# Kernel tuning notes

Hardware: AMD Instinct MI355X
Metric: run time of the kernel (lower is better)

The kernel has to match this reference:

```python
import jax, jax.numpy as jnp
import numpy as np

EPS = 1e-12  # torch F.normalize default eps


def setup_inputs() -> dict:
    key = jax.random.key(0)
    k1, k2, k3, k4, k5 = jax.random.split(key, 5)
    N, E, D_IN, D_OUT = 100000, 1600000, 128, 128
    features = jax.random.normal(k1, (N, D_IN), dtype=jnp.float32)
    W = jax.random.normal(k2, (D_OUT, D_IN), dtype=jnp.float32) * 0.05
    b = jax.random.normal(k3, (D_OUT,), dtype=jnp.float32) * 0.05
    src = jax.random.randint(k4, (E,), 0, N, dtype=jnp.int32)
    dst = jax.random.randint(k5, (E,), 0, N, dtype=jnp.int32)
    return {"features": features, "W": W, "b": b, "src": src, "dst": dst}


def reference(features, W, b, src, dst):
    N = features.shape[0]
    # sum of features over each node's neighbors: scatter-add messages to dst
    neigh_sum = jax.ops.segment_sum(features[src], dst, num_segments=N)  # [N, D]
    total = jnp.sum(features, axis=0)  # [D]
    # non-neighbor sum (excl. self) + self feature == total - neighbor_sum
    h_NN = total[None, :] - neigh_sum  # [N, D]
    # row-wise L2 normalize (torch F.normalize dim=1)
    norm = jnp.sqrt(jnp.sum(h_NN * h_NN, axis=1, keepdims=True))
    h_norm = h_NN / jnp.maximum(norm, EPS)
    # linear: x @ W.T + b
    return h_norm @ W.T + b
```

## Files before the change

kernel.cpp:

```cpp
#include <hip/hip_runtime.h>
#include <hip/hip_bf16.h>

#define D 128

typedef __bf16 bf16_t;
typedef bf16_t bf16x8 __attribute__((ext_vector_type(8)));
typedef float  f32x4  __attribute__((ext_vector_type(4)));
typedef float  f32x2  __attribute__((ext_vector_type(2)));

__device__ __forceinline__ void atomAddF(float* p, float v) {
    unsafeAtomicAdd(p, v);
}

__device__ __forceinline__ uint2 pack_fp8x8(const float* v) {
    unsigned lo = 0, hi = 0;
    lo = __builtin_amdgcn_cvt_pk_fp8_f32(v[0], v[1], lo, false);
    lo = __builtin_amdgcn_cvt_pk_fp8_f32(v[2], v[3], lo, true);
    hi = __builtin_amdgcn_cvt_pk_fp8_f32(v[4], v[5], hi, false);
    hi = __builtin_amdgcn_cvt_pk_fp8_f32(v[6], v[7], hi, true);
    return make_uint2(lo, hi);
}

__device__ __forceinline__ void acc_fp8x8(uint2 w, float* acc) {
    f32x2 a = __builtin_amdgcn_cvt_pk_f32_fp8(w.x, false);
    f32x2 b = __builtin_amdgcn_cvt_pk_f32_fp8(w.x, true);
    f32x2 c = __builtin_amdgcn_cvt_pk_f32_fp8(w.y, false);
    f32x2 d = __builtin_amdgcn_cvt_pk_f32_fp8(w.y, true);
    acc[0] += a[0]; acc[1] += a[1]; acc[2] += b[0]; acc[3] += b[1];
    acc[4] += c[0]; acc[5] += c[1]; acc[6] += d[0]; acc[7] += d[1];
}

__global__ __launch_bounds__(256) void cvt_colsum_count_kernel(const float* __restrict__ feat,
                                                               uint2* __restrict__ featq,
                                                               float* __restrict__ total,
                                                               const int* __restrict__ dst,
                                                               int* __restrict__ bcount,
                                                               long long n8, int nE, int NB) {
    __shared__ float red[4][16][8];
    __shared__ int hist[1024];
    int tid = threadIdx.x, lane = tid & 63, w = tid >> 6;
    for (int i = tid; i < NB; i += 256) hist[i] = 0;
    __syncthreads();
    long long G = (long long)gridDim.x * 256;
    float acc[8];
    #pragma unroll
    for (int e = 0; e < 8; ++e) acc[e] = 0.f;
    long long lim = n8 > (long long)nE ? n8 : (long long)nE;
    for (long long i = (long long)blockIdx.x * 256 + tid; i < lim; i += G) {
        if (i < n8) {
            const float4 a = *(const float4*)&feat[i * 8];
            const float4 b = *(const float4*)&feat[i * 8 + 4];
            float v[8] = {a.x, a.y, a.z, a.w, b.x, b.y, b.z, b.w};
            featq[i] = pack_fp8x8(v);
            acc[0] += a.x; acc[1] += a.y; acc[2] += a.z; acc[3] += a.w;
            acc[4] += b.x; acc[5] += b.y; acc[6] += b.z; acc[7] += b.w;
        }
        if (i < (long long)nE) atomicAdd(&hist[dst[i] >> 8], 1);
    }
    #pragma unroll
    for (int e = 0; e < 8; ++e) {
        acc[e] += __shfl_xor(acc[e], 16, 64);
        acc[e] += __shfl_xor(acc[e], 32, 64);
    }
    if (lane < 16) {
        #pragma unroll
        for (int e = 0; e < 8; ++e) red[w][lane][e] = acc[e];
    }
    __syncthreads();
    if (tid < 128) {
        int cb = tid >> 3, e = tid & 7;
        float s = red[0][cb][e] + red[1][cb][e] + red[2][cb][e] + red[3][cb][e];
        atomAddF(&total[cb * 8 + e], s);
    }
    for (int i = tid; i < NB; i += 256) {
        int h = hist[i];
        if (h) atomicAdd(&bcount[i], h);
    }
}

__global__ __launch_bounds__(1024) void bscan_kernel(const int* __restrict__ bcount,
                                                     int* __restrict__ bbase,
                                                     int* __restrict__ bcur,
                                                     int NB, int nE) {
    int tid = threadIdx.x, lane = tid & 63, w = tid >> 6;
    int v = (tid < NB) ? bcount[tid] : 0;
    int x = v;
    #pragma unroll
    for (int off = 1; off < 64; off <<= 1) {
        int y = __shfl_up(x, off, 64);
        if (lane >= off) x += y;
    }
    __shared__ int ws[16];
    if (lane == 63) ws[w] = x;
    __syncthreads();
    if (w == 0 && lane < 16) {
        int s = ws[lane];
        #pragma unroll
        for (int off = 1; off < 16; off <<= 1) {
            int y = __shfl_up(s, off, 64);
            if (lane >= off) s += y;
        }
        ws[lane] = s;
    }
    __syncthreads();
    int base = (w == 0) ? 0 : ws[w - 1];
    int excl = base + x - v;
    if (tid < NB) { bbase[tid] = excl; bcur[tid] = excl; }
    if (tid == 0) bbase[NB] = nE;
}

__global__ __launch_bounds__(256) void bucket_scatter_kernel(const int* __restrict__ src,
                                                             const int* __restrict__ dst,
                                                             int* __restrict__ bcur,
                                                             unsigned* __restrict__ packed,
                                                             int nE, int NB, int chunk) {
    __shared__ int hist[1024];
    __shared__ int cur[1024];
    int tid = threadIdx.x;
    int c0 = blockIdx.x * chunk;
    int c1 = c0 + chunk; if (c1 > nE) c1 = nE;
    for (int i = tid; i < NB; i += 256) hist[i] = 0;
    __syncthreads();
    for (int i = c0 + tid; i < c1; i += 256) atomicAdd(&hist[dst[i] >> 8], 1);
    __syncthreads();
    for (int i = tid; i < NB; i += 256) {
        int h = hist[i];
        cur[i] = h ? atomicAdd(&bcur[i], h) : 0;
    }
    __syncthreads();
    for (int i = c0 + tid; i < c1; i += 256) {
        int t = dst[i];
        int b = t >> 8;
        int off = atomicAdd(&cur[b], 1);
        packed[off] = ((unsigned)(t & 255) << 17) | (unsigned)src[i];
    }
}

__global__ __launch_bounds__(512) void fill_sort_kernel(const unsigned* __restrict__ packed,
                                                        const int* __restrict__ bbase,
                                                        int* __restrict__ ptr,
                                                        int* __restrict__ adj,
                                                        int n, int NB, int nE) {
    __shared__ int cnt[256];
    __shared__ int lcur[256];
    __shared__ int wsum[4];
    int b = blockIdx.x;
    int tid = threadIdx.x, lane = tid & 63, w = tid >> 6;
    int base = bbase[b], end = bbase[b + 1];
    if (tid < 256) cnt[tid] = 0;
    __syncthreads();
    for (int i = base + tid; i < end; i += 512)
        atomicAdd(&cnt[packed[i] >> 17], 1);
    __syncthreads();
    int v = 0, x = 0;
    if (tid < 256) {
        v = cnt[tid];
        x = v;
        #pragma unroll
        for (int off = 1; off < 64; off <<= 1) {
            int y = __shfl_up(x, off, 64);
            if (lane >= off) x += y;
        }
        if (lane == 63) wsum[w] = x;
    }
    __syncthreads();
    if (tid < 256) {
        int wb = 0;
        for (int k = 0; k < w; ++k) wb += wsum[k];
        int excl = wb + x - v;
        int start = base + excl;
        lcur[tid] = start;
        int node = b * 256 + tid;
        if (node < n) ptr[node] = start;
    }
    if (b == NB - 1 && tid == 0) ptr[n] = nE;
    __syncthreads();
    for (int i = base + tid; i < end; i += 512) {
        unsigned pv = packed[i];
        int j = (int)(pv >> 17);
        int pos = atomicAdd(&lcur[j], 1);
        adj[pos] = (int)(pv & 0x1FFFFu);
    }
}

__global__ __launch_bounds__(256, 4) void gather_mfma_kernel(const uint2* __restrict__ featq,
                                                             const int* __restrict__ ptr,
                                                             const int* __restrict__ adj,
                                                             const float* __restrict__ total,
                                                             const float* __restrict__ W,
                                                             const float* __restrict__ bias,
                                                             float* __restrict__ out,
                                                             int n, int ngroups) {
    __shared__ bf16_t s_hn[2][16][136];

    int tid  = threadIdx.x;
    int lane = tid & 63;
    int w    = tid >> 6;
    int quad = lane >> 4;
    int l16  = lane & 15;

    int n0 = w * 32;
    bf16x8 bfrag[4][2];
    #pragma unroll
    for (int s = 0; s < 4; ++s)
        #pragma unroll
        for (int c = 0; c < 2; ++c) {
            const float* wp = W + (size_t)(n0 + 16 * c + l16) * D + 32 * s + 8 * quad;
            float4 wa = *(const float4*)wp;
            float4 wb = *(const float4*)(wp + 4);
            bf16x8 bf;
            bf[0] = (bf16_t)wa.x; bf[1] = (bf16_t)wa.y; bf[2] = (bf16_t)wa.z; bf[3] = (bf16_t)wa.w;
            bf[4] = (bf16_t)wb.x; bf[5] = (bf16_t)wb.y; bf[6] = (bf16_t)wb.z; bf[7] = (bf16_t)wb.w;
            bfrag[s][c] = bf;
        }
    float bias0 = bias[n0 + l16];
    float bias1 = bias[n0 + 16 + l16];

    int k_node = tid >> 4;
    int d8 = (tid & 15) * 8;
    float tot8[8];
    {
        float4 ta = *(const float4*)&total[d8];
        float4 tb = *(const float4*)&total[d8 + 4];
        tot8[0] = ta.x; tot8[1] = ta.y; tot8[2] = ta.z; tot8[3] = ta.w;
        tot8[4] = tb.x; tot8[5] = tb.y; tot8[6] = tb.z; tot8[7] = tb.w;
    }

    const uint2* fb = featq + (tid & 15);
    int pb = 0;

    for (int g = blockIdx.x; g < ngroups; g += gridDim.x) {
        int v = g * 16 + k_node;
        bool valid = v < n;
        int p0 = valid ? ptr[v] : 0;
        int p1 = valid ? ptr[v + 1] : 0;

        float acc8[8];
        #pragma unroll
        for (int e = 0; e < 8; ++e) acc8[e] = 0.f;

        for (int p = p0; p < p1; p += 16) {
            int rem = p1 - p;
            uint2 f[16];
            #pragma unroll
            for (int i = 0; i < 16; ++i) {
                int q = (i < rem) ? (p + i) : (p1 - 1);
                f[i] = fb[(size_t)adj[q] * 16];
            }
            #pragma unroll
            for (int i = 0; i < 16; ++i) {
                if (i < rem) acc_fp8x8(f[i], acc8);
            }
        }

        float h8[8], ss = 0.f;
        #pragma unroll
        for (int e = 0; e < 8; ++e) {
            h8[e] = valid ? (tot8[e] - acc8[e]) : 0.f;
            ss = fmaf(h8[e], h8[e], ss);
        }
        ss += __shfl_xor(ss, 1, 64);
        ss += __shfl_xor(ss, 2, 64);
        ss += __shfl_xor(ss, 4, 64);
        ss += __shfl_xor(ss, 8, 64);
        float rinv = 1.0f / fmaxf(sqrtf(ss), 1e-12f);

        bf16x8 hv;
        #pragma unroll
        for (int e = 0; e < 8; ++e) hv[e] = (bf16_t)(h8[e] * rinv);
        *(bf16x8*)&s_hn[pb][k_node][d8] = hv;
        __syncthreads();

        f32x4 acc0 = {0.f, 0.f, 0.f, 0.f};
        f32x4 acc1 = {0.f, 0.f, 0.f, 0.f};
        #pragma unroll
        for (int s = 0; s < 4; ++s) {
            bf16x8 a = *(const bf16x8*)&s_hn[pb][l16][32 * s + 8 * quad];
            acc0 = __builtin_amdgcn_mfma_f32_16x16x32_bf16(a, bfrag[s][0], acc0, 0, 0, 0);
            acc1 = __builtin_amdgcn_mfma_f32_16x16x32_bf16(a, bfrag[s][1], acc1, 0, 0, 0);
        }
        #pragma unroll
        for (int r = 0; r < 4; ++r) {
            int row = quad * 4 + r;
            int vr = g * 16 + row;
            if (vr < n) {
                out[(size_t)vr * D + n0 + l16]      = acc0[r] + bias0;
                out[(size_t)vr * D + n0 + 16 + l16] = acc1[r] + bias1;
            }
        }
        pb ^= 1;
    }
}

__global__ __launch_bounds__(128) void col_sum_kernel(const float* __restrict__ feat,
                                                      float* __restrict__ total, int n) {
    int d = threadIdx.x;
    float acc = 0.f;
    for (int r = blockIdx.x; r < n; r += gridDim.x)
        acc += feat[(size_t)r * D + d];
    atomAddF(&total[d], acc);
}

__global__ __launch_bounds__(256) void scatter_kernel(const float* __restrict__ feat,
                                                      const int* __restrict__ src,
                                                      const int* __restrict__ dst,
                                                      float* __restrict__ neigh, int nE) {
    long long nwork = (long long)nE * 64;
    long long stride = (long long)gridDim.x * 256;
    for (long long i = (long long)blockIdx.x * 256 + threadIdx.x; i < nwork; i += stride) {
        int e = (int)(i >> 6);
        int d2 = (int)(i & 63) * 2;
        int s = src[e], t = dst[e];
        const float2 vv = *(const float2*)&feat[(size_t)s * D + d2];
        float* p = &neigh[(size_t)t * D + d2];
        atomAddF(p + 0, vv.x);
        atomAddF(p + 1, vv.y);
    }
}

__global__ __launch_bounds__(256) void finalize_kernel(const float* __restrict__ neigh,
                                                       const float* __restrict__ total,
                                                       const float* __restrict__ W,
                                                       const float* __restrict__ bias,
                                                       float* __restrict__ out,
                                                       int n, int ngroups) {
    __shared__ __hip_bfloat16 Wt[D * D];
    __shared__ __align__(16) float hnt[2][D][4];
    __shared__ float red[2][2][4];
    int tid = threadIdx.x;
    for (int idx = tid; idx < D * D; idx += 256) {
        int j = idx & 127, dd = idx >> 7;
        Wt[idx] = __float2bfloat16(W[(size_t)j * D + dd]);
    }
    int half = tid >> 7, d = tid & 127, wih = (tid >> 6) & 1, lane = tid & 63;
    float bj = bias[d], tot = total[d];
    __syncthreads();
    for (int g = blockIdx.x; g < ngroups; g += gridDim.x) {
        int nb = g * 8 + half * 4;
        float h0=0,h1=0,h2=0,h3=0;
        if (nb+0 < n) h0 = tot - neigh[(size_t)(nb+0)*D + d];
        if (nb+1 < n) h1 = tot - neigh[(size_t)(nb+1)*D + d];
        if (nb+2 < n) h2 = tot - neigh[(size_t)(nb+2)*D + d];
        if (nb+3 < n) h3 = tot - neigh[(size_t)(nb+3)*D + d];
        float s0=h0*h0,s1=h1*h1,s2=h2*h2,s3=h3*h3;
        #pragma unroll
        for (int off = 32; off > 0; off >>= 1) {
            s0 += __shfl_xor(s0, off, 64); s1 += __shfl_xor(s1, off, 64);
            s2 += __shfl_xor(s2, off, 64); s3 += __shfl_xor(s3, off, 64);
        }
        if (lane == 0) { red[half][wih][0]=s0; red[half][wih][1]=s1; red[half][wih][2]=s2; red[half][wih][3]=s3; }
        __syncthreads();
        float rinv[4];
        #pragma unroll
        for (int k = 0; k < 4; ++k)
            rinv[k] = 1.0f / fmaxf(sqrtf(red[half][0][k] + red[half][1][k]), 1e-12f);
        hnt[half][d][0]=h0*rinv[0]; hnt[half][d][1]=h1*rinv[1];
        hnt[half][d][2]=h2*rinv[2]; hnt[half][d][3]=h3*rinv[3];
        __syncthreads();
        float a0=0,a1=0,a2=0,a3=0;
        #pragma unroll 8
        for (int dd = 0; dd < D; ++dd) {
            float4 hn4 = *(const float4*)&hnt[half][dd][0];
            float wv = __bfloat162float(Wt[dd * D + d]);
            a0 = fmaf(hn4.x, wv, a0); a1 = fmaf(hn4.y, wv, a1);
            a2 = fmaf(hn4.z, wv, a2); a3 = fmaf(hn4.w, wv, a3);
        }
        if (nb+0 < n) out[(size_t)(nb+0)*D + d] = a0 + bj;
        if (nb+1 < n) out[(size_t)(nb+1)*D + d] = a1 + bj;
        if (nb+2 < n) out[(size_t)(nb+2)*D + d] = a2 + bj;
        if (nb+3 < n) out[(size_t)(nb+3)*D + d] = a3 + bj;
        __syncthreads();
    }
}

static inline size_t align_up(size_t x, size_t a) { return (x + a - 1) & ~(a - 1); }

extern "C" void kernel_launch(void* const* d_in, const int* in_sizes, int n_in,
                              void* d_out, int out_size, void* d_ws, size_t ws_size,
                              hipStream_t stream) {
    const float* feat = (const float*)d_in[0];
    const float* W    = (const float*)d_in[1];
    const float* bias = (const float*)d_in[2];
    const int*   src  = (const int*)d_in[3];
    const int*   dst  = (const int*)d_in[4];
    float* out = (float*)d_out;

    int n  = in_sizes[0] / D;
    int nE = in_sizes[3];
    int NB = (n + 255) / 256;

    char* wsb = (char*)d_ws;
    size_t o_total  = 0;
    size_t o_bcount = 512;
    size_t o_bbase  = o_bcount + 4096;
    size_t o_bcur   = o_bbase + 4608;
    size_t o_ptr    = o_bcur + 4096;
    size_t o_adj    = align_up(o_ptr + (size_t)4 * (n + 1), 512);
    size_t o_packed = o_adj + (size_t)4 * nE;
    size_t o_featq  = align_up(o_packed + (size_t)4 * nE, 512);
    size_t needNew  = o_featq + (size_t)n * D;

    float*    total  = (float*)(wsb + o_total);
    int*      bcount = (int*)(wsb + o_bcount);
    int*      bbase  = (int*)(wsb + o_bbase);
    int*      bcur   = (int*)(wsb + o_bcur);
    int*      ptr    = (int*)(wsb + o_ptr);
    int*      adj    = (int*)(wsb + o_adj);
    unsigned* packed = (unsigned*)(wsb + o_packed);
    uint2*    featq  = (uint2*)(wsb + o_featq);

    long long n8 = (long long)n * (D / 8);
    int ngroups16 = (n + 15) / 16;
    int grid16 = (ngroups16 + 2) / 3;
    if (grid16 > 4096) grid16 = 4096;

    bool packOK = (n <= (1 << 17)) && (NB <= 1024);

    if (ws_size >= needNew && packOK) {
        hipMemsetAsync(wsb, 0, o_bbase, stream);
        cvt_colsum_count_kernel<<<512, 256, 0, stream>>>(feat, featq, total, dst, bcount,
                                                         n8, nE, NB);
        int chunk = (nE + 511) / 512;
        bscan_kernel<<<1, 1024, 0, stream>>>(bcount, bbase, bcur, NB, nE);
        bucket_scatter_kernel<<<512, 256, 0, stream>>>(src, dst, bcur, packed, nE, NB, chunk);
        fill_sort_kernel<<<NB, 512, 0, stream>>>(packed, bbase, ptr, adj, n, NB, nE);
        gather_mfma_kernel<<<grid16, 256, 0, stream>>>(featq, ptr, adj, total, W, bias,
                                                       out, n, ngroups16);
    } else {
        float* neigh = out;
        if (ws_size >= D * sizeof(float))
            hipMemsetAsync(d_ws, 0, D * sizeof(float), stream);
        hipMemsetAsync(neigh, 0, (size_t)out_size * sizeof(float), stream);
        col_sum_kernel<<<512, 128, 0, stream>>>(feat, total, n);
        scatter_kernel<<<16384, 256, 0, stream>>>(feat, src, dst, neigh, nE);
        int ngroups = (n + 7) / 8;
        finalize_kernel<<<2048, 256, 0, stream>>>(neigh, total, W, bias, out, n, ngroups);
    }
}
```

Baseline: 234.5 us.

## Reuse per-chunk dst histograms, prebuild bf16 W fragments, shuffle adjacency loads

The count kernel now walks the same contiguous edge chunks as the scatter kernel and stores each block's bucket histogram, so the scatter kernel no longer re-reads dst to recount. The bscan kernel also converts W into bf16 MFMA fragment order once, and the gather kernel loads those fragments per tile instead of keeping them in registers, which lowers register pressure. In the gather loop, each lane loads one adjacency index and broadcasts it with shuffles instead of every lane reading all sixteen. fill_sort switches to 1024-thread blocks. The cost is an extra 2 MB histogram buffer and reloading W fragments for every tile.

```diff
diff --git a/kernel.cpp b/kernel.cpp
--- a/kernel.cpp
+++ b/kernel.cpp
@@ -35,7 +35,9 @@
                                                                float* __restrict__ total,
                                                                const int* __restrict__ dst,
                                                                int* __restrict__ bcount,
-                                                               long long n8, int nE, int NB) {
+                                                               int* __restrict__ chunkhist,
+                                                               long long n8, int nE, int NB,
+                                                               int chunk) {
     __shared__ float red[4][16][8];
     __shared__ int hist[1024];
     int tid = threadIdx.x, lane = tid & 63, w = tid >> 6;
@@ -45,8 +47,11 @@
     float acc[8];
     #pragma unroll
     for (int e = 0; e < 8; ++e) acc[e] = 0.f;
-    long long lim = n8 > (long long)nE ? n8 : (long long)nE;
-    for (long long i = (long long)blockIdx.x * 256 + tid; i < lim; i += G) {
+    int c0 = blockIdx.x * chunk;
+    int c1 = c0 + chunk; if (c1 > nE) c1 = nE;
+    long long i = (long long)blockIdx.x * 256 + tid;
+    int e = c0 + tid;
+    while (i < n8 || e < c1) {
         if (i < n8) {
             const float4 a = *(const float4*)&feat[i * 8];
             const float4 b = *(const float4*)&feat[i * 8 + 4];
@@ -55,32 +60,37 @@
             acc[0] += a.x; acc[1] += a.y; acc[2] += a.z; acc[3] += a.w;
             acc[4] += b.x; acc[5] += b.y; acc[6] += b.z; acc[7] += b.w;
         }
-        if (i < (long long)nE) atomicAdd(&hist[dst[i] >> 8], 1);
+        if (e < c1) atomicAdd(&hist[dst[e] >> 8], 1);
+        i += G; e += 256;
     }
     #pragma unroll
-    for (int e = 0; e < 8; ++e) {
-        acc[e] += __shfl_xor(acc[e], 16, 64);
-        acc[e] += __shfl_xor(acc[e], 32, 64);
+    for (int k = 0; k < 8; ++k) {
+        acc[k] += __shfl_xor(acc[k], 16, 64);
+        acc[k] += __shfl_xor(acc[k], 32, 64);
     }
     if (lane < 16) {
         #pragma unroll
-        for (int e = 0; e < 8; ++e) red[w][lane][e] = acc[e];
+        for (int k = 0; k < 8; ++k) red[w][lane][k] = acc[k];
     }
     __syncthreads();
     if (tid < 128) {
-        int cb = tid >> 3, e = tid & 7;
-        float s = red[0][cb][e] + red[1][cb][e] + red[2][cb][e] + red[3][cb][e];
-        atomAddF(&total[cb * 8 + e], s);
-    }
-    for (int i = tid; i < NB; i += 256) {
-        int h = hist[i];
-        if (h) atomicAdd(&bcount[i], h);
+        int cb = tid >> 3, k = tid & 7;
+        float s = red[0][cb][k] + red[1][cb][k] + red[2][cb][k] + red[3][cb][k];
+        atomAddF(&total[cb * 8 + k], s);
+    }
+    int* ch = chunkhist + (size_t)blockIdx.x * 1024;
+    for (int k = tid; k < NB; k += 256) {
+        int h = hist[k];
+        ch[k] = h;
+        if (h) atomicAdd(&bcount[k], h);
     }
 }
 
 __global__ __launch_bounds__(1024) void bscan_kernel(const int* __restrict__ bcount,
                                                      int* __restrict__ bbase,
                                                      int* __restrict__ bcur,
+                                                     const float* __restrict__ W,
+                                                     bf16x8* __restrict__ fragbuf,
                                                      int NB, int nE) {
     int tid = threadIdx.x, lane = tid & 63, w = tid >> 6;
     int v = (tid < NB) ? bcount[tid] : 0;
@@ -107,27 +117,39 @@
     int excl = base + x - v;
     if (tid < NB) { bbase[tid] = excl; bcur[tid] = excl; }
     if (tid == 0) bbase[NB] = nE;
+
+    for (int fidx = tid; fidx < 2048; fidx += 1024) {
+        int t  = fidx >> 3, fi = fidx & 7;
+        int tw = t >> 6, quad = (t >> 4) & 3, l16 = t & 15;
+        int s  = fi >> 1, c = fi & 1;
+        int row = tw * 32 + 16 * c + l16;
+        int col = 32 * s + 8 * quad;
+        const float* wp = W + (size_t)row * D + col;
+        float4 wa = *(const float4*)wp;
+        float4 wb = *(const float4*)(wp + 4);
+        bf16x8 bf;
+        bf[0] = (bf16_t)wa.x; bf[1] = (bf16_t)wa.y; bf[2] = (bf16_t)wa.z; bf[3] = (bf16_t)wa.w;
+        bf[4] = (bf16_t)wb.x; bf[5] = (bf16_t)wb.y; bf[6] = (bf16_t)wb.z; bf[7] = (bf16_t)wb.w;
+        fragbuf[fidx] = bf;
+    }
 }
 
 __global__ __launch_bounds__(256) void bucket_scatter_kernel(const int* __restrict__ src,
                                                              const int* __restrict__ dst,
                                                              int* __restrict__ bcur,
                                                              unsigned* __restrict__ packed,
+                                                             const int* __restrict__ chunkhist,
                                                              int nE, int NB, int chunk) {
-    __shared__ int hist[1024];
     __shared__ int cur[1024];
     int tid = threadIdx.x;
+    const int* ch = chunkhist + (size_t)blockIdx.x * 1024;
+    for (int i = tid; i < NB; i += 256) {
+        int h = ch[i];
+        cur[i] = h ? atomicAdd(&bcur[i], h) : 0;
+    }
+    __syncthreads();
     int c0 = blockIdx.x * chunk;
     int c1 = c0 + chunk; if (c1 > nE) c1 = nE;
-    for (int i = tid; i < NB; i += 256) hist[i] = 0;
-    __syncthreads();
-    for (int i = c0 + tid; i < c1; i += 256) atomicAdd(&hist[dst[i] >> 8], 1);
-    __syncthreads();
-    for (int i = tid; i < NB; i += 256) {
-        int h = hist[i];
-        cur[i] = h ? atomicAdd(&bcur[i], h) : 0;
-    }
-    __syncthreads();
     for (int i = c0 + tid; i < c1; i += 256) {
         int t = dst[i];
         int b = t >> 8;
@@ -136,11 +158,11 @@
     }
 }
 
-__global__ __launch_bounds__(512) void fill_sort_kernel(const unsigned* __restrict__ packed,
-                                                        const int* __restrict__ bbase,
-                                                        int* __restrict__ ptr,
-                                                        int* __restrict__ adj,
-                                                        int n, int NB, int nE) {
+__global__ __launch_bounds__(1024) void fill_sort_kernel(const unsigned* __restrict__ packed,
+                                                         const int* __restrict__ bbase,
+                                                         int* __restrict__ ptr,
+                                                         int* __restrict__ adj,
+                                                         int n, int NB, int nE) {
     __shared__ int cnt[256];
     __shared__ int lcur[256];
     __shared__ int wsum[4];
@@ -149,7 +171,7 @@
     int base = bbase[b], end = bbase[b + 1];
     if (tid < 256) cnt[tid] = 0;
     __syncthreads();
-    for (int i = base + tid; i < end; i += 512)
+    for (int i = base + tid; i < end; i += 1024)
         atomicAdd(&cnt[packed[i] >> 17], 1);
     __syncthreads();
     int v = 0, x = 0;
@@ -175,7 +197,7 @@
     }
     if (b == NB - 1 && tid == 0) ptr[n] = nE;
     __syncthreads();
-    for (int i = base + tid; i < end; i += 512) {
+    for (int i = base + tid; i < end; i += 1024) {
         unsigned pv = packed[i];
         int j = (int)(pv >> 17);
         int pos = atomicAdd(&lcur[j], 1);
@@ -187,7 +209,7 @@
                                                              const int* __restrict__ ptr,
                                                              const int* __restrict__ adj,
                                                              const float* __restrict__ total,
-                                                             const float* __restrict__ W,
+                                                             const bf16x8* __restrict__ fragbuf,
                                                              const float* __restrict__ bias,
                                                              float* __restrict__ out,
                                                              int n, int ngroups) {
@@ -200,19 +222,6 @@
     int l16  = lane & 15;
 
     int n0 = w * 32;
-    bf16x8 bfrag[4][2];
-    #pragma unroll
-    for (int s = 0; s < 4; ++s)
-        #pragma unroll
-        for (int c = 0; c < 2; ++c) {
-            const float* wp = W + (size_t)(n0 + 16 * c + l16) * D + 32 * s + 8 * quad;
-            float4 wa = *(const float4*)wp;
-            float4 wb = *(const float4*)(wp + 4);
-            bf16x8 bf;
-            bf[0] = (bf16_t)wa.x; bf[1] = (bf16_t)wa.y; bf[2] = (bf16_t)wa.z; bf[3] = (bf16_t)wa.w;
-            bf[4] = (bf16_t)wb.x; bf[5] = (bf16_t)wb.y; bf[6] = (bf16_t)wb.z; bf[7] = (bf16_t)wb.w;
-            bfrag[s][c] = bf;
-        }
     float bias0 = bias[n0 + l16];
     float bias1 = bias[n0 + 16 + l16];
 
@@ -227,6 +236,7 @@
     }
 
     const uint2* fb = featq + (tid & 15);
+    uintptr_t fragp = (uintptr_t)(fragbuf + (size_t)tid * 8);
     int pb = 0;
 
     for (int g = blockIdx.x; g < ngroups; g += gridDim.x) {
@@ -241,12 +251,16 @@
 
         for (int p = p0; p < p1; p += 16) {
             int rem = p1 - p;
+            int q = p + l16; if (q > p1 - 1) q = p1 - 1;
+            int myadj = adj[q];
             uint2 f[16];
             #pragma unroll
             for (int i = 0; i < 16; ++i) {
-                int q = (i < rem) ? (p + i) : (p1 - 1);
-                f[i] = fb[(size_t)adj[q] * 16];
+                int idx = __shfl(myadj, (lane & 48) + i, 64);
+                f[i] = fb[(size_t)idx * 16];
             }
+            #pragma unroll
+            for (int i = 0; i < 16; ++i) asm volatile("" :: "v"(f[i]));
             #pragma unroll
             for (int i = 0; i < 16; ++i) {
                 if (i < rem) acc_fp8x8(f[i], acc8);
@@ -271,13 +285,19 @@
         *(bf16x8*)&s_hn[pb][k_node][d8] = hv;
         __syncthreads();
 
+        uintptr_t fp_ = fragp;
+        asm volatile("" : "+v"(fp_));
+        const bf16x8* fg = (const bf16x8*)fp_;
+
         f32x4 acc0 = {0.f, 0.f, 0.f, 0.f};
         f32x4 acc1 = {0.f, 0.f, 0.f, 0.f};
         #pragma unroll
         for (int s = 0; s < 4; ++s) {
-            bf16x8 a = *(const bf16x8*)&s_hn[pb][l16][32 * s + 8 * quad];
-            acc0 = __builtin_amdgcn_mfma_f32_16x16x32_bf16(a, bfrag[s][0], acc0, 0, 0, 0);
-            acc1 = __builtin_amdgcn_mfma_f32_16x16x32_bf16(a, bfrag[s][1], acc1, 0, 0, 0);
+            bf16x8 a  = *(const bf16x8*)&s_hn[pb][l16][32 * s + 8 * quad];
+            bf16x8 b0 = fg[2 * s];
+            bf16x8 b1 = fg[2 * s + 1];
+            acc0 = __builtin_amdgcn_mfma_f32_16x16x32_bf16(a, b0, acc0, 0, 0, 0);
+            acc1 = __builtin_amdgcn_mfma_f32_16x16x32_bf16(a, b1, acc1, 0, 0, 0);
         }
         #pragma unroll
         for (int r = 0; r < 4; ++r) {
@@ -392,9 +412,11 @@
     char* wsb = (char*)d_ws;
     size_t o_total  = 0;
     size_t o_bcount = 512;
-    size_t o_bbase  = o_bcount + 4096;
+    size_t o_bbase  = 4608;
     size_t o_bcur   = o_bbase + 4608;
-    size_t o_ptr    = o_bcur + 4096;
+    size_t o_chist  = align_up(o_bcur + 4096, 512);
+    size_t o_frag   = o_chist + (size_t)512 * 1024 * 4;
+    size_t o_ptr    = o_frag + 2048 * 16;
     size_t o_adj    = align_up(o_ptr + (size_t)4 * (n + 1), 512);
     size_t o_packed = o_adj + (size_t)4 * nE;
     size_t o_featq  = align_up(o_packed + (size_t)4 * nE, 512);
@@ -404,6 +426,8 @@
     int*      bcount = (int*)(wsb + o_bcount);
     int*      bbase  = (int*)(wsb + o_bbase);
     int*      bcur   = (int*)(wsb + o_bcur);
+    int*      chist  = (int*)(wsb + o_chist);
+    bf16x8*   fragbuf= (bf16x8*)(wsb + o_frag);
     int*      ptr    = (int*)(wsb + o_ptr);
     int*      adj    = (int*)(wsb + o_adj);
     unsigned* packed = (unsigned*)(wsb + o_packed);
@@ -418,14 +442,15 @@
 
     if (ws_size >= needNew && packOK) {
         hipMemsetAsync(wsb, 0, o_bbase, stream);
+        int chunk = (nE + 511) / 512;
         cvt_colsum_count_kernel<<<512, 256, 0, stream>>>(feat, featq, total, dst, bcount,
-                                                         n8, nE, NB);
-        int chunk = (nE + 511) / 512;
-        bscan_kernel<<<1, 1024, 0, stream>>>(bcount, bbase, bcur, NB, nE);
-        bucket_scatter_kernel<<<512, 256, 0, stream>>>(src, dst, bcur, packed, nE, NB, chunk);
-        fill_sort_kernel<<<NB, 512, 0, stream>>>(packed, bbase, ptr, adj, n, NB, nE);
-        gather_mfma_kernel<<<grid16, 256, 0, stream>>>(featq, ptr, adj, total, W, bias,
-                                                       out, n, ngroups16);
+                                                         chist, n8, nE, NB, chunk);
+        bscan_kernel<<<1, 1024, 0, stream>>>(bcount, bbase, bcur, W, fragbuf, NB, nE);
+        bucket_scatter_kernel<<<512, 256, 0, stream>>>(src, dst, bcur, packed, chist,
+                                                       nE, NB, chunk);
+        fill_sort_kernel<<<NB, 1024, 0, stream>>>(packed, bbase, ptr, adj, n, NB, nE);
+        gather_mfma_kernel<<<grid16, 256, 0, stream>>>(featq, ptr, adj, total, fragbuf,
+                                                       bias, out, n, ngroups16);
     } else {
         float* neigh = out;
         if (ws_size >= D * sizeof(float))
```

New measurement: 242.8 us. 1.04x slower.

## Build CSR via per-node counts and direct atomic scatter; prefetch adjacency in gather

Applied to the files above, without the earlier changes.

Replaces the two-level bucket sort (bucket scatter plus in-bucket fill sort through a packed buffer) with per-node degree counting during the conversion pass, a per-bucket node scan, and a direct global-atomic scatter of src into adj. This removes one full pass over the edges and the packed intermediate, but adds 1.6M global atomics on ncount and ncur, and the adjacency order within a node becomes nondeterministic. The gather kernel also now loads adjacency indices once per 16-lane group and broadcasts them by shuffle. It uses inline-asm loads with split waitcnts and prefetches the next group's ptr and adj values to overlap latency.

```diff
diff --git a/kernel.cpp b/kernel.cpp
--- a/kernel.cpp
+++ b/kernel.cpp
@@ -35,6 +35,7 @@
                                                                float* __restrict__ total,
                                                                const int* __restrict__ dst,
                                                                int* __restrict__ bcount,
+                                                               int* __restrict__ ncount,
                                                                long long n8, int nE, int NB) {
     __shared__ float red[4][16][8];
     __shared__ int hist[1024];
@@ -55,32 +56,35 @@
             acc[0] += a.x; acc[1] += a.y; acc[2] += a.z; acc[3] += a.w;
             acc[4] += b.x; acc[5] += b.y; acc[6] += b.z; acc[7] += b.w;
         }
-        if (i < (long long)nE) atomicAdd(&hist[dst[i] >> 8], 1);
+        if (i < (long long)nE) {
+            int t = dst[i];
+            atomicAdd(&hist[t >> 8], 1);
+            atomicAdd(&ncount[t], 1);
+        }
     }
     #pragma unroll
-    for (int e = 0; e < 8; ++e) {
-        acc[e] += __shfl_xor(acc[e], 16, 64);
-        acc[e] += __shfl_xor(acc[e], 32, 64);
+    for (int k = 0; k < 8; ++k) {
+        acc[k] += __shfl_xor(acc[k], 16, 64);
+        acc[k] += __shfl_xor(acc[k], 32, 64);
     }
     if (lane < 16) {
         #pragma unroll
-        for (int e = 0; e < 8; ++e) red[w][lane][e] = acc[e];
+        for (int k = 0; k < 8; ++k) red[w][lane][k] = acc[k];
     }
     __syncthreads();
     if (tid < 128) {
-        int cb = tid >> 3, e = tid & 7;
-        float s = red[0][cb][e] + red[1][cb][e] + red[2][cb][e] + red[3][cb][e];
-        atomAddF(&total[cb * 8 + e], s);
-    }
-    for (int i = tid; i < NB; i += 256) {
-        int h = hist[i];
-        if (h) atomicAdd(&bcount[i], h);
+        int cb = tid >> 3, k = tid & 7;
+        float s = red[0][cb][k] + red[1][cb][k] + red[2][cb][k] + red[3][cb][k];
+        atomAddF(&total[cb * 8 + k], s);
+    }
+    for (int k = tid; k < NB; k += 256) {
+        int h = hist[k];
+        if (h) atomicAdd(&bcount[k], h);
     }
 }
 
 __global__ __launch_bounds__(1024) void bscan_kernel(const int* __restrict__ bcount,
                                                      int* __restrict__ bbase,
-                                                     int* __restrict__ bcur,
                                                      int NB, int nE) {
     int tid = threadIdx.x, lane = tid & 63, w = tid >> 6;
     int v = (tid < NB) ? bcount[tid] : 0;
@@ -105,81 +109,43 @@
     __syncthreads();
     int base = (w == 0) ? 0 : ws[w - 1];
     int excl = base + x - v;
-    if (tid < NB) { bbase[tid] = excl; bcur[tid] = excl; }
+    if (tid < NB) bbase[tid] = excl;
     if (tid == 0) bbase[NB] = nE;
 }
 
-__global__ __launch_bounds__(256) void bucket_scatter_kernel(const int* __restrict__ src,
+__global__ __launch_bounds__(256) void nscan_kernel(const int* __restrict__ ncount,
+                                                    const int* __restrict__ bbase,
+                                                    int* __restrict__ ptr,
+                                                    int* __restrict__ ncur,
+                                                    int n, int NB, int nE) {
+    __shared__ int wsum[4];
+    int b = blockIdx.x, tid = threadIdx.x, lane = tid & 63, w = tid >> 6;
+    int v = b * 256 + tid;
+    int c = (v < n) ? ncount[v] : 0;
+    int x = c;
+    #pragma unroll
+    for (int off = 1; off < 64; off <<= 1) {
+        int y = __shfl_up(x, off, 64);
+        if (lane >= off) x += y;
+    }
+    if (lane == 63) wsum[w] = x;
+    __syncthreads();
+    int wb = 0;
+    for (int k = 0; k < w; ++k) wb += wsum[k];
+    int p = bbase[b] + wb + x - c;
+    if (v < n) { ptr[v] = p; ncur[v] = p; }
+    if (b == NB - 1 && tid == 255) ptr[n] = nE;
+}
+
+__global__ __launch_bounds__(256) void scatter_direct_kernel(const int* __restrict__ src,
                                                              const int* __restrict__ dst,
-                                                             int* __restrict__ bcur,
-                                                             unsigned* __restrict__ packed,
-                                                             int nE, int NB, int chunk) {
-    __shared__ int hist[1024];
-    __shared__ int cur[1024];
-    int tid = threadIdx.x;
-    int c0 = blockIdx.x * chunk;
-    int c1 = c0 + chunk; if (c1 > nE) c1 = nE;
-    for (int i = tid; i < NB; i += 256) hist[i] = 0;
-    __syncthreads();
-    for (int i = c0 + tid; i < c1; i += 256) atomicAdd(&hist[dst[i] >> 8], 1);
-    __syncthreads();
-    for (int i = tid; i < NB; i += 256) {
-        int h = hist[i];
-        cur[i] = h ? atomicAdd(&bcur[i], h) : 0;
-    }
-    __syncthreads();
-    for (int i = c0 + tid; i < c1; i += 256) {
+                                                             int* __restrict__ ncur,
+                                                             int* __restrict__ adj, int nE) {
+    int stride = gridDim.x * 256;
+    for (int i = blockIdx.x * 256 + threadIdx.x; i < nE; i += stride) {
         int t = dst[i];
-        int b = t >> 8;
-        int off = atomicAdd(&cur[b], 1);
-        packed[off] = ((unsigned)(t & 255) << 17) | (unsigned)src[i];
-    }
-}
-
-__global__ __launch_bounds__(512) void fill_sort_kernel(const unsigned* __restrict__ packed,
-                                                        const int* __restrict__ bbase,
-                                                        int* __restrict__ ptr,
-                                                        int* __restrict__ adj,
-                                                        int n, int NB, int nE) {
-    __shared__ int cnt[256];
-    __shared__ int lcur[256];
-    __shared__ int wsum[4];
-    int b = blockIdx.x;
-    int tid = threadIdx.x, lane = tid & 63, w = tid >> 6;
-    int base = bbase[b], end = bbase[b + 1];
-    if (tid < 256) cnt[tid] = 0;
-    __syncthreads();
-    for (int i = base + tid; i < end; i += 512)
-        atomicAdd(&cnt[packed[i] >> 17], 1);
-    __syncthreads();
-    int v = 0, x = 0;
-    if (tid < 256) {
-        v = cnt[tid];
-        x = v;
-        #pragma unroll
-        for (int off = 1; off < 64; off <<= 1) {
-            int y = __shfl_up(x, off, 64);
-            if (lane >= off) x += y;
-        }
-        if (lane == 63) wsum[w] = x;
-    }
-    __syncthreads();
-    if (tid < 256) {
-        int wb = 0;
-        for (int k = 0; k < w; ++k) wb += wsum[k];
-        int excl = wb + x - v;
-        int start = base + excl;
-        lcur[tid] = start;
-        int node = b * 256 + tid;
-        if (node < n) ptr[node] = start;
-    }
-    if (b == NB - 1 && tid == 0) ptr[n] = nE;
-    __syncthreads();
-    for (int i = base + tid; i < end; i += 512) {
-        unsigned pv = packed[i];
-        int j = (int)(pv >> 17);
-        int pos = atomicAdd(&lcur[j], 1);
-        adj[pos] = (int)(pv & 0x1FFFFu);
+        int pos = atomicAdd(&ncur[t], 1);
+        adj[pos] = src[i];
     }
 }
 
@@ -226,33 +192,59 @@
         tot8[4] = tb.x; tot8[5] = tb.y; tot8[6] = tb.z; tot8[7] = tb.w;
     }
 
-    const uint2* fb = featq + (tid & 15);
+    unsigned sliceoff = (unsigned)(tid & 15) * 8;
+    unsigned long long fbase = (unsigned long long)featq;
     int pb = 0;
-
-    for (int g = blockIdx.x; g < ngroups; g += gridDim.x) {
+    int gstride = gridDim.x;
+    int g = blockIdx.x;
+
+    int p0 = 0, p1 = 0, madj = 0;
+    if (g < ngroups) {
+        int v = g * 16 + k_node;
+        if (v < n) { p0 = ptr[v]; p1 = ptr[v + 1]; }
+        if (p0 < p1) { int q = p0 + l16; if (q > p1 - 1) q = p1 - 1; madj = adj[q]; }
+    }
+
+    for (; g < ngroups; g += gstride) {
+        int gn = g + gstride;
+        int np0 = 0, np1 = 0;
+        if (gn < ngroups) {
+            int vn = gn * 16 + k_node;
+            if (vn < n) { np0 = ptr[vn]; np1 = ptr[vn + 1]; }
+        }
+
+        float acc8[8];
+        #pragma unroll
+        for (int e = 0; e < 8; ++e) acc8[e] = 0.f;
+
+        for (int p = p0; p < p1; p += 16) {
+            int rem = p1 - p;
+            unsigned voff[16];
+            #pragma unroll
+            for (int i = 0; i < 16; ++i) {
+                int idx = __shfl(madj, (lane & 48) + i, 64);
+                voff[i] = ((unsigned)idx << 7) | sliceoff;
+            }
+            uint2 f[16];
+            #pragma unroll
+            for (int i = 0; i < 16; ++i)
+                asm volatile("global_load_dwordx2 %0, %1, %2"
+                             : "=v"(f[i]) : "v"(voff[i]), "s"(fbase));
+            int adjn = 0, pn = p + 16;
+            if (pn < p1) { int q = pn + l16; if (q > p1 - 1) q = p1 - 1; adjn = adj[q]; }
+            asm volatile("s_waitcnt vmcnt(8)" ::: "memory");
+            __builtin_amdgcn_sched_barrier(0);
+            #pragma unroll
+            for (int i = 0; i < 8; ++i) if (i < rem) acc_fp8x8(f[i], acc8);
+            asm volatile("s_waitcnt vmcnt(0)" ::: "memory");
+            __builtin_amdgcn_sched_barrier(0);
+            #pragma unroll
+            for (int i = 8; i < 16; ++i) if (i < rem) acc_fp8x8(f[i], acc8);
+            madj = adjn;
+        }
+
         int v = g * 16 + k_node;
         bool valid = v < n;
-        int p0 = valid ? ptr[v] : 0;
-        int p1 = valid ? ptr[v + 1] : 0;
-
-        float acc8[8];
-        #pragma unroll
-        for (int e = 0; e < 8; ++e) acc8[e] = 0.f;
-
-        for (int p = p0; p < p1; p += 16) {
-            int rem = p1 - p;
-            uint2 f[16];
-            #pragma unroll
-            for (int i = 0; i < 16; ++i) {
-                int q = (i < rem) ? (p + i) : (p1 - 1);
-                f[i] = fb[(size_t)adj[q] * 16];
-            }
-            #pragma unroll
-            for (int i = 0; i < 16; ++i) {
-                if (i < rem) acc_fp8x8(f[i], acc8);
-            }
-        }
-
         float h8[8], ss = 0.f;
         #pragma unroll
         for (int e = 0; e < 8; ++e) {
@@ -270,6 +262,9 @@
         for (int e = 0; e < 8; ++e) hv[e] = (bf16_t)(h8[e] * rinv);
         *(bf16x8*)&s_hn[pb][k_node][d8] = hv;
         __syncthreads();
+
+        p0 = np0; p1 = np1; madj = 0;
+        if (p0 < p1) { int q = p0 + l16; if (q > p1 - 1) q = p1 - 1; madj = adj[q]; }
 
         f32x4 acc0 = {0.f, 0.f, 0.f, 0.f};
         f32x4 acc1 = {0.f, 0.f, 0.f, 0.f};
@@ -392,40 +387,39 @@
     char* wsb = (char*)d_ws;
     size_t o_total  = 0;
     size_t o_bcount = 512;
-    size_t o_bbase  = o_bcount + 4096;
-    size_t o_bcur   = o_bbase + 4608;
-    size_t o_ptr    = o_bcur + 4096;
-    size_t o_adj    = align_up(o_ptr + (size_t)4 * (n + 1), 512);
-    size_t o_packed = o_adj + (size_t)4 * nE;
-    size_t o_featq  = align_up(o_packed + (size_t)4 * nE, 512);
+    size_t o_ncount = 512 + 4096;
+    size_t o_bbase  = align_up(o_ncount + (size_t)4 * n, 512);
+    size_t o_ptr    = align_up(o_bbase + (size_t)4 * (NB + 1), 512);
+    size_t o_ncur   = align_up(o_ptr + (size_t)4 * (n + 1), 512);
+    size_t o_adj    = align_up(o_ncur + (size_t)4 * n, 512);
+    size_t o_featq  = align_up(o_adj + (size_t)4 * nE, 512);
     size_t needNew  = o_featq + (size_t)n * D;
 
-    float*    total  = (float*)(wsb + o_total);
-    int*      bcount = (int*)(wsb + o_bcount);
-    int*      bbase  = (int*)(wsb + o_bbase);
-    int*      bcur   = (int*)(wsb + o_bcur);
-    int*      ptr    = (int*)(wsb + o_ptr);
-    int*      adj    = (int*)(wsb + o_adj);
-    unsigned* packed = (unsigned*)(wsb + o_packed);
-    uint2*    featq  = (uint2*)(wsb + o_featq);
+    float* total  = (float*)(wsb + o_total);
+    int*   bcount = (int*)(wsb + o_bcount);
+    int*   ncount = (int*)(wsb + o_ncount);
+    int*   bbase  = (int*)(wsb + o_bbase);
+    int*   ptr    = (int*)(wsb + o_ptr);
+    int*   ncur   = (int*)(wsb + o_ncur);
+    int*   adj    = (int*)(wsb + o_adj);
+    uint2* featq  = (uint2*)(wsb + o_featq);
 
     long long n8 = (long long)n * (D / 8);
     int ngroups16 = (n + 15) / 16;
     int grid16 = (ngroups16 + 2) / 3;
     if (grid16 > 4096) grid16 = 4096;
 
-    bool packOK = (n <= (1 << 17)) && (NB <= 1024);
+    bool packOK = (NB <= 1024);
 
     if (ws_size >= needNew && packOK) {
         hipMemsetAsync(wsb, 0, o_bbase, stream);
-        cvt_colsum_count_kernel<<<512, 256, 0, stream>>>(feat, featq, total, dst, bcount,
-                                                         n8, nE, NB);
-        int chunk = (nE + 511) / 512;
-        bscan_kernel<<<1, 1024, 0, stream>>>(bcount, bbase, bcur, NB, nE);
-        bucket_scatter_kernel<<<512, 256, 0, stream>>>(src, dst, bcur, packed, nE, NB, chunk);
-        fill_sort_kernel<<<NB, 512, 0, stream>>>(packed, bbase, ptr, adj, n, NB, nE);
-        gather_mfma_kernel<<<grid16, 256, 0, stream>>>(featq, ptr, adj, total, W, bias,
-                                                       out, n, ngroups16);
+        cvt_colsum_count_kernel<<<512, 256, 0, stream>>>(feat, featq, total, dst,
+                                                         bcount, ncount, n8, nE, NB);
+        bscan_kernel<<<1, 1024, 0, stream>>>(bcount, bbase, NB, nE);
+        nscan_kernel<<<NB, 256, 0, stream>>>(ncount, bbase, ptr, ncur, n, NB, nE);
+        scatter_direct_kernel<<<1024, 256, 0, stream>>>(src, dst, ncur, adj, nE);
+        gather_mfma_kernel<<<grid16, 256, 0, stream>>>(featq, ptr, adj, total, W,
+                                                       bias, out, n, ngroups16);
     } else {
         float* neigh = out;
         if (ws_size >= D * sizeof(float))
```

Result: slower. 362.7 us (+54.6%).
